# Kernel tuning notes

Hardware: AMD Instinct MI355X
Metric: run time of the kernel (lower is better)

## Reference

```python
import jax, jax.numpy as jnp
import numpy as np

N_NODES = 20000
N_EDGES = 240000
NUM_SPECIES = 4
NUM_BASIS = 16
MAX_RADIUS = 3.15
SQRT_NN = float(np.sqrt(12.0))  # num_neighbors normalization


def _cg121():
    # Clebsch-Gordan for 1e x 2e -> 1e in the real l=2 basis used below:
    # [xy, yz, (3z^2-1), zx, x^2-y^2] (component-normalized). Built from the
    # symmetric traceless matrix pairing M(a) @ v, normalized to unit Frobenius norm.
    s5, s15 = np.sqrt(5.0), np.sqrt(15.0)
    C = np.zeros((3, 5, 3))
    for A in range(5):
        a = np.zeros(5); a[A] = 1.0
        M = np.zeros((3, 3))
        M[0, 1] = M[1, 0] = a[0] * s15 / 2
        M[1, 2] = M[2, 1] = a[1] * s15 / 2
        M[0, 2] = M[2, 0] = a[3] * s15 / 2
        M[0, 0] = -a[2] * s5 / 2 + a[4] * s15 / 2
        M[1, 1] = -a[2] * s5 / 2 - a[4] * s15 / 2
        M[2, 2] = a[2] * s5
        C[:, A, :] = M
    C /= np.linalg.norm(C)
    return jnp.asarray(C, dtype=jnp.float32)

CG121 = _cg121()


def silu(v):
    return v * jax.nn.sigmoid(v)


def lin0(h, W):  # equivariant linear on scalars: [N,u] x [u,v]
    return h @ W / np.sqrt(W.shape[0])


def lin1(h, W):  # equivariant linear on vectors: [N,u,3] x [u,v]
    return jnp.einsum('nuk,uv->nvk', h, W) / np.sqrt(W.shape[0])


def radial_mlp(hb, W1, W2):  # FullyConnectedNet([16,64,nw], silu), normalized weights
    h = silu(hb @ W1 / np.sqrt(W1.shape[0]))
    return h @ W2 / np.sqrt(W2.shape[0])


def radial_basis(r):
    # soft_one_hot_linspace(..., basis='smooth_finite', cutoff=True) * sqrt(NUM_BASIS)
    values = np.linspace(0.0, MAX_RADIUS, NUM_BASIS + 2, dtype=np.float32)[1:-1]
    step = float(values[1] - values[0])
    d = (r[:, None] - values) / step
    def sus(t):
        safe = jnp.where(t > 0, t, 1.0)
        return jnp.where(t > 0, jnp.exp(-1.0 / safe), 0.0)
    y = 1.14136 * float(np.exp(2.0)) * sus(1.0 + d) * sus(1.0 - d)
    return y * np.sqrt(float(NUM_BASIS))


def sph_harm(edge_vec):
    # normalize=True, normalization='component' real spherical harmonics, l=0,1,2
    r = jnp.linalg.norm(edge_vec, axis=1)
    u = edge_vec / r[:, None]
    ux, uy, uz = u[:, 0], u[:, 1], u[:, 2]
    sh1 = np.sqrt(3.0) * u
    sh2 = jnp.stack([np.sqrt(15.0) * ux * uy,
                     np.sqrt(15.0) * uy * uz,
                     np.sqrt(5.0) / 2 * (3 * uz * uz - 1.0),
                     np.sqrt(15.0) * uz * ux,
                     np.sqrt(15.0) / 2 * (ux * ux - uy * uy)], axis=1)
    return r, sh1, sh2


def _forward(x, edge_index, edge_vec, emb,
             L1_lin1_0, L1_W1, L1_W2, L1_lin2_0, L1_lin2_1, L1_sc_0,
             L2_lin1_0, L2_lin1_1, L2_W1, L2_W2, L2_lin2_0, L2_lin2_1, L2_sc_0, L2_sc_1,
             LO_lin1_0, LO_lin1_1, LO_W1, LO_W2, LO_lin2_0, LO_sc_0):
    src, dst = edge_index[0], edge_index[1]
    N = x.shape[0]
    h0 = emb[x]                                   # [N,64] node embedding
    r, sh1, sh2 = sph_harm(edge_vec)
    hb = radial_basis(r)                          # [E,16]

    # ---- interaction 1: 64x0e -> (144x0e + 16x1e) -> gate -> 128x0e + 16x1e
    sc0 = lin0(h0, L1_sc_0)                       # self-connection [N,144]
    x0 = lin0(h0, L1_lin1_0)[src]                 # [E,64]
    w = radial_mlp(hb, L1_W1, L1_W2)              # [E,128] TP weights (uvu)
    m0 = x0 * w[:, :64]                           # 0e x 0e -> 0e
    m1 = (x0 * w[:, 64:128])[:, :, None] * sh1[:, None, :]  # 0e x 1e -> 1e
    a0 = jax.ops.segment_sum(m0, dst, num_segments=N) / SQRT_NN
    a1 = jax.ops.segment_sum(m1, dst, num_segments=N) / SQRT_NN
    g0 = lin0(a0, L1_lin2_0) + sc0                # [N,144]
    g1 = lin1(a1, L1_lin2_1)                      # [N,16,3]
    h0 = silu(g0[:, :128])                        # gated scalars
    h1 = jax.nn.sigmoid(g0[:, 128:])[:, :, None] * g1  # gate 16x1e

    # ---- interaction 2: 128x0e+16x1e -> (144x0e + 176x1e mid) -> gate
    sc0 = lin0(h0, L2_sc_0)                       # [N,144]
    sc1 = lin1(h1, L2_sc_1)                       # [N,16,3]
    x0 = lin0(h0, L2_lin1_0)[src]                 # [E,128]
    x1 = lin1(h1, L2_lin1_1)[src]                 # [E,16,3]
    w = radial_mlp(hb, L2_W1, L2_W2)              # [E,320]
    m0a = x0 * w[:, :128]                                            # 0x0->0
    m0b = jnp.einsum('euk,ek->eu', x1, sh1) / np.sqrt(3.0) * w[:, 272:288]  # 1x1->0
    m1a = (x0 * w[:, 128:256])[:, :, None] * sh1[:, None, :]         # 0x1->1
    m1b = x1 * w[:, 256:272][:, :, None]                             # 1x0->1
    m1c = jnp.cross(x1, sh1[:, None, :]) / np.sqrt(6.0) * w[:, 288:304][:, :, None]  # 1x1->1
    m1d = jnp.einsum('eui,eA,iAk->euk', x1, sh2, CG121) * w[:, 304:320][:, :, None]  # 1x2->1
    mid0 = jnp.concatenate([m0a, m0b], axis=1)    # [E,144]
    mid1 = jnp.concatenate([m1a, m1b, m1c, m1d], axis=1)  # [E,176,3]
    a0 = jax.ops.segment_sum(mid0, dst, num_segments=N) / SQRT_NN
    a1 = jax.ops.segment_sum(mid1, dst, num_segments=N) / SQRT_NN
    g0 = lin0(a0, L2_lin2_0) + sc0
    g1 = lin1(a1, L2_lin2_1) + sc1
    h0 = silu(g0[:, :128])
    h1 = jax.nn.sigmoid(g0[:, 128:])[:, :, None] * g1

    # ---- output interaction: -> 4x0e
    sc0 = lin0(h0, LO_sc_0)                       # [N,4]
    x0 = lin0(h0, LO_lin1_0)[src]
    x1 = lin1(h1, LO_lin1_1)[src]
    w = radial_mlp(hb, LO_W1, LO_W2)              # [E,144]
    m0a = x0 * w[:, :128]
    m0b = jnp.einsum('euk,ek->eu', x1, sh1) / np.sqrt(3.0) * w[:, 128:144]
    a0 = jax.ops.segment_sum(jnp.concatenate([m0a, m0b], axis=1), dst, num_segments=N) / SQRT_NN
    return lin0(a0, LO_lin2_0) + sc0              # [N,4]


def setup_inputs() -> dict:
    key = jax.random.key(0)
    ks = jax.random.split(key, 32)
    f = lambda i, shape: jax.random.normal(ks[i], shape, dtype=jnp.float32)
    return {
        'x': jax.random.randint(ks[0], (N_NODES,), 0, NUM_SPECIES),
        'edge_index': jax.random.randint(ks[1], (2, N_EDGES), 0, N_NODES),
        'edge_vec': jax.random.normal(ks[2], (N_EDGES, 3), dtype=jnp.float32),
        'emb': f(3, (NUM_SPECIES, 64)),
        'L1_lin1_0': f(4, (64, 64)),
        'L1_W1': f(5, (16, 64)), 'L1_W2': f(6, (64, 128)),
        'L1_lin2_0': f(7, (64, 144)), 'L1_lin2_1': f(8, (64, 16)),
        'L1_sc_0': f(9, (64, 144)),
        'L2_lin1_0': f(10, (128, 128)), 'L2_lin1_1': f(11, (16, 16)),
        'L2_W1': f(12, (16, 64)), 'L2_W2': f(13, (64, 320)),
        'L2_lin2_0': f(14, (144, 144)), 'L2_lin2_1': f(15, (176, 16)),
        'L2_sc_0': f(16, (128, 144)), 'L2_sc_1': f(17, (16, 16)),
        'LO_lin1_0': f(18, (128, 128)), 'LO_lin1_1': f(19, (16, 16)),
        'LO_W1': f(20, (16, 64)), 'LO_W2': f(21, (64, 144)),
        'LO_lin2_0': f(22, (144, 4)), 'LO_sc_0': f(23, (128, 4)),
    }


def reference(x, edge_index, edge_vec, emb,
              L1_lin1_0, L1_W1, L1_W2, L1_lin2_0, L1_lin2_1, L1_sc_0,
              L2_lin1_0, L2_lin1_1, L2_W1, L2_W2, L2_lin2_0, L2_lin2_1, L2_sc_0, L2_sc_1,
              LO_lin1_0, LO_lin1_1, LO_W1, LO_W2, LO_lin2_0, LO_sc_0):
    return _forward(x, edge_index, edge_vec, emb,
                    L1_lin1_0, L1_W1, L1_W2, L1_lin2_0, L1_lin2_1, L1_sc_0,
                    L2_lin1_0, L2_lin1_1, L2_W1, L2_W2, L2_lin2_0, L2_lin2_1, L2_sc_0, L2_sc_1,
                    LO_lin1_0, LO_lin1_1, LO_W1, LO_W2, LO_lin2_0, LO_sc_0)
```

## Files before the change

### kernel.cpp

```cpp
#include <hip/hip_runtime.h>
#include <math.h>

#define N_NODES 20000
#define N_EDGES 240000

typedef _Float16 half2_t __attribute__((ext_vector_type(2)));
typedef _Float16 f16x8   __attribute__((ext_vector_type(8)));
typedef float    f32x4v  __attribute__((ext_vector_type(4)));
typedef unsigned uint4v  __attribute__((ext_vector_type(4)));

__device__ __forceinline__ float siluf(float v){ return v * (1.0f/(1.0f+__expf(-v))); }
__device__ __forceinline__ float sigmf(float v){ return 1.0f/(1.0f+__expf(-v)); }

__device__ __forceinline__ unsigned pack_h2(float a, float b){
  half2_t h; h.x = (_Float16)a; h.y = (_Float16)b;
  return __builtin_bit_cast(unsigned, h);
}
__device__ __forceinline__ float dot2f(unsigned w, unsigned h, float acc){
#if __has_builtin(__builtin_amdgcn_fdot2)
  return __builtin_amdgcn_fdot2(__builtin_bit_cast(half2_t,w),
                                __builtin_bit_cast(half2_t,h), acc, false);
#else
  half2_t a = __builtin_bit_cast(half2_t,w), b = __builtin_bit_cast(half2_t,h);
  return acc + (float)a.x*(float)b.x + (float)a.y*(float)b.y;
#endif
}

__global__ void k_count(const int* __restrict__ ei, int* __restrict__ cnt){
  int e = blockIdx.x*blockDim.x + threadIdx.x;
  if (e < N_EDGES) atomicAdd(&cnt[ei[N_EDGES + e]], 1);
}

__global__ void k_scan(const int* __restrict__ cnt, int* __restrict__ off, int* __restrict__ pos){
  __shared__ int part[1024];
  int t = threadIdx.x;
  int c[20]; int s = 0;
  #pragma unroll
  for (int j=0;j<20;j++){
    int idx = t*20 + j;
    int v = (idx < N_NODES) ? cnt[idx] : 0;
    c[j] = s; s += v;
  }
  part[t] = s;
  __syncthreads();
  for (int d=1; d<1024; d<<=1){
    int add = (t>=d) ? part[t-d] : 0;
    __syncthreads();
    part[t] += add;
    __syncthreads();
  }
  int excl = part[t] - s;
  #pragma unroll
  for (int j=0;j<20;j++){
    int idx = t*20 + j;
    if (idx < N_NODES){ off[idx] = excl + c[j]; pos[idx] = excl + c[j]; }
  }
  if (t == 1023) off[N_NODES] = part[1023];
}

__global__ void k_scatter(const int* __restrict__ ei, int* __restrict__ pos,
                          int* __restrict__ perm, int* __restrict__ srcs){
  int e = blockIdx.x*blockDim.x + threadIdx.x;
  if (e >= N_EDGES) return;
  int d = ei[N_EDGES + e];
  int p = atomicAdd(&pos[d], 1);
  perm[e] = p;
  srcs[p] = ei[e];
}

__global__ void k_geom(const float* __restrict__ ev, const int* __restrict__ perm,
                       float* __restrict__ eg){
  int e = blockIdx.x*blockDim.x + threadIdx.x;
  if (e >= N_EDGES) return;
  float x = ev[3*e+0], y = ev[3*e+1], z = ev[3*e+2];
  float r = sqrtf(x*x + y*y + z*z);
  float inv = 1.0f / fmaxf(r, 1e-12f);
  float ux = x*inv, uy = y*inv, uz = z*inv;
  float* o = eg + (size_t)perm[e]*24;
  o[0] = 1.7320508f*ux; o[1] = 1.7320508f*uy; o[2] = 1.7320508f*uz;
  o[3] = 3.8729833f*ux*uy;
  o[4] = 3.8729833f*uy*uz;
  o[5] = 1.1180340f*(3.0f*uz*uz - 1.0f);
  o[6] = 3.8729833f*uz*ux;
  o[7] = 1.9364917f*(ux*ux - uy*uy);
  const float invstep = 17.0f/3.15f;
  float t = r*invstep;
  #pragma unroll
  for (int i=0;i<16;i++){
    float d = t - (float)(i+1);
    float a = 1.0f + d, b = 1.0f - d;
    float v = 0.0f;
    if (a > 0.0f && b > 0.0f) v = 33.734292f*__expf(-1.0f/a - 1.0f/b);
    o[8+i] = v;
  }
}

__global__ void k_packw(const float* __restrict__ W20, const float* __restrict__ Wsc0,
                        const float* __restrict__ Wl0,
                        unsigned* __restrict__ WPu, unsigned* __restrict__ WPs,
                        unsigned* __restrict__ WPl){
  int i = blockIdx.x*blockDim.x + threadIdx.x;
  const float f12 = 1.0f/12.0f;
  const float is128 = 0.08838835f;
  if (i < 144*72){
    int t = i/72, k2 = i%72;
    WPu[i] = pack_h2(W20[(2*k2)*144+t]*f12, W20[(2*k2+1)*144+t]*f12);
  } else if (i < 144*72 + 144*64){
    int ii = i - 144*72; int t = ii/64, k2 = ii%64;
    WPs[ii] = pack_h2(Wsc0[(2*k2)*144+t]*is128, Wsc0[(2*k2+1)*144+t]*is128);
  } else if (i < 144*72 + 144*64 + 128*64){
    int ii = i - 144*72 - 144*64; int t = ii/64, k2 = ii%64;
    WPl[ii] = pack_h2(Wl0[(2*k2)*128+t]*is128, Wl0[(2*k2+1)*128+t]*is128);
  }
}

__global__ void k_node_l1(const int* __restrict__ xs, const float* __restrict__ emb,
                          const float* __restrict__ Wlin, const float* __restrict__ Wsc,
                          float* __restrict__ X0, float* __restrict__ SC0){
  __shared__ float hs[4][64];
  int n0 = blockIdx.x*4;
  int t  = threadIdx.x;
  {
    int j = t>>6, k = t&63;
    hs[j][k] = emb[xs[n0+j]*64 + k];
  }
  __syncthreads();
  if (t < 64){
    float acc[4] = {};
    for (int k=0;k<64;k++){
      float wv = Wlin[k*64 + t];
      #pragma unroll
      for (int j=0;j<4;j++) acc[j] += hs[j][k]*wv;
    }
    #pragma unroll
    for (int j=0;j<4;j++) X0[(size_t)(n0+j)*64 + t] = acc[j]*0.125f;
  } else if (t < 208){
    int o = t - 64;
    float acc[4] = {};
    for (int k=0;k<64;k++){
      float wv = Wsc[k*144 + o];
      #pragma unroll
      for (int j=0;j<4;j++) acc[j] += hs[j][k]*wv;
    }
    #pragma unroll
    for (int j=0;j<4;j++) SC0[(size_t)(n0+j)*144 + o] = acc[j]*0.125f;
  }
}

__global__ __launch_bounds__(256) void k_hidden(
    const float* __restrict__ EG, const float* __restrict__ W1,
    _Float16* __restrict__ H){
  __shared__ float w1s[16*64];
  int tid = threadIdx.x;
  for (int i=tid;i<16*64;i+=256) w1s[i] = W1[i]*0.25f;
  __syncthreads();
  int lane = tid & 63, wib = tid >> 6;
  int gw = blockIdx.x*4 + wib, nw = gridDim.x*4;
  for (int e = gw; e < N_EDGES; e += nw){
    const float* g8 = EG + (size_t)e*24 + 8;
    float a0 = 0.0f, a1 = 0.0f;
    #pragma unroll
    for (int b=0;b<8;b++){
      a0 = fmaf(g8[b],   w1s[b*64 + lane],     a0);
      a1 = fmaf(g8[8+b], w1s[(8+b)*64 + lane], a1);
    }
    H[(size_t)e*64 + lane] = (_Float16)siluf(a0 + a1);
  }
}

template<int MODE>
__device__ __forceinline__ float colscale(int c){
  if constexpr (MODE == 1){
    if (c >= 272 && c < 288) return 0.57735027f;
    if (c >= 288 && c < 304) return 0.40824829f;
    return 1.0f;
  } else if constexpr (MODE == 2){
    return (c >= 128) ? 0.57735027f : 1.0f;
  }
  return 1.0f;
}

template<int NT, int MODE>
__global__ __launch_bounds__(256) void k_ww_mfma(
    int e0c, int e1c, const _Float16* __restrict__ H,
    const float* __restrict__ W2, _Float16* __restrict__ WW){
  constexpr int NCOL = NT*16;
  constexpr int NTW  = (NT + 3) / 4;
  int tid = threadIdx.x;
  int lane = tid & 63, wib = tid >> 6;
  int row = lane & 15, quad = lane >> 4;
  const float fold = 0.125f*0.28867513f;
  f16x8 B0[NTW], B1[NTW];
  #pragma unroll
  for (int t2=0; t2<NTW; t2++){
    int ct = wib*NTW + t2;
    int c  = ct*16 + row;
    bool valid = (ct < NT);
    float fs = valid ? fold*colscale<MODE>(c) : 0.0f;
    int ci = valid ? c : 0;
    #pragma unroll
    for (int j=0;j<8;j++){
      B0[t2][j] = (_Float16)(W2[(quad*8+j)*NCOL + ci]*fs);
      B1[t2][j] = (_Float16)(W2[(32+quad*8+j)*NCOL + ci]*fs);
    }
  }
  int ntiles = (e1c - e0c) >> 4;
  for (int t = blockIdx.x; t < ntiles; t += gridDim.x){
    int eb = e0c + t*16;
    const _Float16* hp = H + (size_t)(eb + row)*64 + quad*8;
    f16x8 A0 = *(const f16x8*)hp;
    f16x8 A1 = *(const f16x8*)(hp + 32);
    #pragma unroll
    for (int t2=0; t2<NTW; t2++){
      int ct = wib*NTW + t2;
      f32x4v d = __builtin_amdgcn_mfma_f32_16x16x32_f16(A0, B0[t2], (f32x4v){0.f,0.f,0.f,0.f}, 0,0,0);
      d = __builtin_amdgcn_mfma_f32_16x16x32_f16(A1, B1[t2], d, 0,0,0);
      if (ct < NT){
        int c0 = ct*16;
        #pragma unroll
        for (int j=0;j<4;j++){
          WW[(size_t)(eb - e0c + quad*4 + j)*NCOL + c0 + row] = (_Float16)d[j];
        }
      }
    }
  }
}

__global__ __launch_bounds__(256) void k_gather_l1(
    const int* __restrict__ off, const int* __restrict__ srcs, const float* __restrict__ eg,
    const _Float16* __restrict__ WW, const float* __restrict__ X0,
    float* __restrict__ A0, float* __restrict__ A1, int e0, int e1, int first){
  int tid = threadIdx.x, lane = tid & 63;
  int gw = (blockIdx.x*256 + tid) >> 6;
  int nw = (gridDim.x*256) >> 6;
  for (int n = gw; n < N_NODES; n += nw){
    int ib = off[n], ie = off[n+1];
    if (ib < e0) ib = e0;
    if (ie > e1) ie = e1;
    if (!first && ib >= ie) continue;
    float a0a = 0.0f, a1a[3] = {0,0,0};
    for (int i = ib; i < ie; i++){
      const float* g = eg + (size_t)i*24;
      const _Float16* w = WW + (size_t)(i - e0)*128;
      float w0  = (float)w[lane];
      float w1v = (float)w[64 + lane];
      float x0 = X0[(size_t)srcs[i]*64 + lane];
      float m0 = x0*w0, m1 = x0*w1v;
      a0a += m0;
      a1a[0] += m1*g[0]; a1a[1] += m1*g[1]; a1a[2] += m1*g[2];
    }
    float* p = A1 + (size_t)n*192 + lane*3;
    if (first){
      A0[(size_t)n*64 + lane] = a0a;
      p[0] = a1a[0]; p[1] = a1a[1]; p[2] = a1a[2];
    } else {
      A0[(size_t)n*64 + lane] += a0a;
      p[0] += a1a[0]; p[1] += a1a[1]; p[2] += a1a[2];
    }
  }
}

__global__ __launch_bounds__(256) void k_gather_l2(
    const int* __restrict__ off, const int* __restrict__ srcs, const float* __restrict__ eg,
    const _Float16* __restrict__ WW, const float* __restrict__ X0, const float* __restrict__ X1,
    float* __restrict__ A0, float* __restrict__ A1, int e0, int e1, int first){
  int tid = threadIdx.x, lane = tid & 63;
  int grp = lane >> 4, v = lane & 15;
  int gw = (blockIdx.x*256 + tid) >> 6;
  int nw = (gridDim.x*256) >> 6;
  for (int n = gw; n < N_NODES; n += nw){
    int ib = off[n], ie = off[n+1];
    if (ib < e0) ib = e0;
    if (ie > e1) ie = e1;
    if (!first && ib >= ie) continue;
    float a0a=0.f, a0b=0.f, a0c=0.f;
    float a1a[3]={0,0,0}, a1b[3]={0,0,0}, a1g[3]={0,0,0};
    for (int i = ib; i < ie; i++){
      const float* g = eg + (size_t)i*24;
      int src = srcs[i];
      const _Float16* w = WW + (size_t)(i - e0)*320;
      float w0  = (float)w[lane];
      float w1v = (float)w[ 64 + lane];
      float w2v = (float)w[128 + lane];
      float w3v = (float)w[192 + lane];
      float w4  = (float)w[256 + lane];
      const float* x0p = X0 + (size_t)src*128;
      float x0a = x0p[lane], x0b = x0p[64 + lane];
      float sx = g[0], sy = g[1], sz = g[2];
      a0a += x0a*w0;
      a0b += x0b*w1v;
      float ma = x0a*w2v, mb = x0b*w3v;
      a1a[0] += ma*sx; a1a[1] += ma*sy; a1a[2] += ma*sz;
      a1b[0] += mb*sx; a1b[1] += mb*sy; a1b[2] += mb*sz;
      const float* x1p = X1 + (size_t)src*48 + v*3;
      float xx = x1p[0], xy = x1p[1], xz = x1p[2];
      if (grp == 0){
        a1g[0] += w4*xx; a1g[1] += w4*xy; a1g[2] += w4*xz;
      } else if (grp == 1){
        a0c += w4*(xx*sx + xy*sy + xz*sz);
      } else if (grp == 2){
        a1g[0] += w4*(xy*sz - xz*sy);
        a1g[1] += w4*(xz*sx - xx*sz);
        a1g[2] += w4*(xx*sy - xy*sx);
      } else {
        float s20=g[3], s21=g[4], s22=g[5], s23=g[6], s24=g[7];
        const float c1c = 0.31622777f, c2c = 0.18257419f;
        a1g[0] += w4*(xx*(c1c*s24 - c2c*s22) + xy*(c1c*s20)            + xz*(c1c*s23));
        a1g[1] += w4*(xx*(c1c*s20)           + xy*(-c2c*s22 - c1c*s24) + xz*(c1c*s21));
        a1g[2] += w4*(xx*(c1c*s23)           + xy*(c1c*s21)            + xz*(2.0f*c2c*s22));
      }
    }
    float* a0 = A0 + (size_t)n*144;
    float* a1 = A1 + (size_t)n*528;
    int gbase = (grp == 0) ? 128 : (grp == 2) ? 144 : (grp == 3) ? 160 : -1;
    if (first){
      a0[lane] = a0a;
      a0[64 + lane] = a0b;
      if (grp == 1) a0[128 + v] = a0c;
      float* p = a1 + lane*3;
      p[0] = a1a[0]; p[1] = a1a[1]; p[2] = a1a[2];
      p = a1 + (64 + lane)*3;
      p[0] = a1b[0]; p[1] = a1b[1]; p[2] = a1b[2];
      if (gbase >= 0){
        p = a1 + (gbase + v)*3;
        p[0] = a1g[0]; p[1] = a1g[1]; p[2] = a1g[2];
      }
    } else {
      a0[lane] += a0a;
      a0[64 + lane] += a0b;
      if (grp == 1) a0[128 + v] += a0c;
      float* p = a1 + lane*3;
      p[0] += a1a[0]; p[1] += a1a[1]; p[2] += a1a[2];
      p = a1 + (64 + lane)*3;
      p[0] += a1b[0]; p[1] += a1b[1]; p[2] += a1b[2];
      if (gbase >= 0){
        p = a1 + (gbase + v)*3;
        p[0] += a1g[0]; p[1] += a1g[1]; p[2] += a1g[2];
      }
    }
  }
}

__global__ __launch_bounds__(256) void k_gather_lo(
    const int* __restrict__ off, const int* __restrict__ srcs, const float* __restrict__ eg,
    const _Float16* __restrict__ WW, const float* __restrict__ X0, const float* __restrict__ X1,
    float* __restrict__ A0, int e0, int e1, int first){
  int tid = threadIdx.x, lane = tid & 63, v = lane & 15;
  int gw = (blockIdx.x*256 + tid) >> 6;
  int nw = (gridDim.x*256) >> 6;
  for (int n = gw; n < N_NODES; n += nw){
    int ib = off[n], ie = off[n+1];
    if (ib < e0) ib = e0;
    if (ie > e1) ie = e1;
    if (!first && ib >= ie) continue;
    float a0a = 0.f, a0b = 0.f, a0c = 0.f;
    for (int i = ib; i < ie; i++){
      const float* g = eg + (size_t)i*24;
      int src = srcs[i];
      const _Float16* w = WW + (size_t)(i - e0)*144;
      float w0  = (float)w[lane];
      float w1v = (float)w[64 + lane];
      float w2v = (float)w[128 + v];
      const float* x0p = X0 + (size_t)src*128;
      a0a += x0p[lane]*w0;
      a0b += x0p[64 + lane]*w1v;
      const float* x1p = X1 + (size_t)src*48 + v*3;
      float dot = x1p[0]*g[0] + x1p[1]*g[1] + x1p[2]*g[2];
      a0c += w2v*dot;
    }
    float* a0 = A0 + (size_t)n*144;
    if (first){
      a0[lane] = a0a;
      a0[64 + lane] = a0b;
      if (lane < 16) a0[128 + lane] = a0c;
    } else {
      a0[lane] += a0a;
      a0[64 + lane] += a0b;
      if (lane < 16) a0[128 + lane] += a0c;
    }
  }
}

__global__ __launch_bounds__(256) void k_upd_l1(
    const float* __restrict__ A0, const float* __restrict__ A1,
    const float* __restrict__ SC0,
    const float* __restrict__ W20, const float* __restrict__ W21,
    float* __restrict__ H0, float* __restrict__ H1){
  __shared__ float a0s[8*64];
  __shared__ float a1s[8*192];
  __shared__ float sig[8][16];
  __shared__ float g1s[8][48];
  int n0 = blockIdx.x*8, t = threadIdx.x;
  {
    const float4* s0 = (const float4*)(A0 + (size_t)n0*64);
    float4* d0 = (float4*)a0s;
    for (int i=t;i<8*64/4;i+=256) d0[i] = s0[i];
    const float4* s1 = (const float4*)(A1 + (size_t)n0*192);
    float4* d1 = (float4*)a1s;
    for (int i=t;i<8*192/4;i+=256) d1[i] = s1[i];
  }
  __syncthreads();
  if (t < 144){
    float acc[8] = {};
    for (int k=0;k<64;k++){
      float wv = W20[k*144 + t];
      #pragma unroll
      for (int j=0;j<8;j++) acc[j] += a0s[j*64 + k]*wv;
    }
    #pragma unroll
    for (int j=0;j<8;j++){
      float gg = acc[j]*0.125f + SC0[(size_t)(n0+j)*144 + t];
      if (t < 128) H0[(size_t)(n0+j)*128 + t] = siluf(gg);
      else         sig[j][t-128] = sigmf(gg);
    }
  } else if (t < 192){
    int idx = t-144, v = idx/3, k = idx%3;
    float acc[8] = {};
    for (int u=0;u<64;u++){
      float wv = W21[u*16 + v];
      #pragma unroll
      for (int j=0;j<8;j++) acc[j] += a1s[j*192 + u*3 + k]*wv;
    }
    #pragma unroll
    for (int j=0;j<8;j++) g1s[j][idx] = acc[j]*0.125f;
  }
  __syncthreads();
  if (t >= 144 && t < 192){
    int idx = t-144, v = idx/3;
    #pragma unroll
    for (int j=0;j<8;j++) H1[(size_t)(n0+j)*48 + idx] = sig[j][v]*g1s[j][idx];
  }
}

__global__ __launch_bounds__(384) void k_lin_l2(
    const float* __restrict__ H0, const float* __restrict__ H1,
    const unsigned* __restrict__ WPs, const float* __restrict__ Wsc1,
    const unsigned* __restrict__ WPl, const float* __restrict__ Wl1,
    float* __restrict__ SC0, float* __restrict__ SC1,
    float* __restrict__ X0,  float* __restrict__ X1){
  __shared__ uint4v h0h8[128];
  __shared__ float h1s[8*48];
  int n0 = blockIdx.x*8, t = threadIdx.x;
  if (t < 128){
    const float4* s0 = (const float4*)(H0 + (size_t)n0*128);
    float4 f0 = s0[t*2], f1 = s0[t*2+1];
    uint4v u;
    u.x = pack_h2(f0.x, f0.y); u.y = pack_h2(f0.z, f0.w);
    u.z = pack_h2(f1.x, f1.y); u.w = pack_h2(f1.z, f1.w);
    h0h8[t] = u;
  } else if (t < 224){
    int i = t - 128;
    const float4* s1 = (const float4*)(H1 + (size_t)n0*48);
    if (i < 96) ((float4*)h1s)[i] = s1[i];
  }
  __syncthreads();
  const uint4v* wps4 = (const uint4v*)WPs;
  const uint4v* wpl4 = (const uint4v*)WPl;
  if (t < 144){
    float acc[8] = {};
    for (int kq=0;kq<16;kq++){
      uint4v wq = wps4[t*16 + kq];
      #pragma unroll
      for (int j=0;j<8;j++){
        uint4v av = h0h8[j*16 + kq];
        acc[j] = dot2f(wq.x, av.x, acc[j]);
        acc[j] = dot2f(wq.y, av.y, acc[j]);
        acc[j] = dot2f(wq.z, av.z, acc[j]);
        acc[j] = dot2f(wq.w, av.w, acc[j]);
      }
    }
    #pragma unroll
    for (int j=0;j<8;j++) SC0[(size_t)(n0+j)*144 + t] = acc[j];
  } else if (t < 192){
    int idx = t-144, v = idx/3, k = idx%3;
    float acc[8] = {};
    for (int u=0;u<16;u++){
      float wv = Wsc1[u*16 + v];
      #pragma unroll
      for (int j=0;j<8;j++) acc[j] += h1s[j*48 + u*3 + k]*wv;
    }
    #pragma unroll
    for (int j=0;j<8;j++) SC1[(size_t)(n0+j)*48 + idx] = acc[j]*0.25f;
  } else if (t < 320){
    int o = t-192;
    float acc[8] = {};
    for (int kq=0;kq<16;kq++){
      uint4v wq = wpl4[o*16 + kq];
      #pragma unroll
      for (int j=0;j<8;j++){
        uint4v av = h0h8[j*16 + kq];
        acc[j] = dot2f(wq.x, av.x, acc[j]);
        acc[j] = dot2f(wq.y, av.y, acc[j]);
        acc[j] = dot2f(wq.z, av.z, acc[j]);
        acc[j] = dot2f(wq.w, av.w, acc[j]);
      }
    }
    #pragma unroll
    for (int j=0;j<8;j++) X0[(size_t)(n0+j)*128 + o] = acc[j];
  } else if (t < 368){
    int idx = t-320, v = idx/3, k = idx%3;
    float acc[8] = {};
    for (int u=0;u<16;u++){
      float wv = Wl1[u*16 + v];
      #pragma unroll
      for (int j=0;j<8;j++) acc[j] += h1s[j*48 + u*3 + k]*wv;
    }
    #pragma unroll
    for (int j=0;j<8;j++) X1[(size_t)(n0+j)*48 + idx] = acc[j]*0.25f;
  }
}

__global__ __launch_bounds__(256) void k_upd_l2(
    const float* __restrict__ A0, const float* __restrict__ A1,
    const float* __restrict__ SC0, const float* __restrict__ SC1,
    const unsigned* __restrict__ WPu, const float* __restrict__ W21,
    float* __restrict__ H0, float* __restrict__ H1){
  __shared__ uint4v a0h8[144];
  __shared__ float a1s[8*528];
  __shared__ float sig[8][16];
  __shared__ float g1s[8][48];
  int n0 = blockIdx.x*8, t = threadIdx.x;
  if (t < 144){
    const float4* s0 = (const float4*)(A0 + (size_t)n0*144);
    float4 f0 = s0[t*2], f1 = s0[t*2+1];
    uint4v u;
    u.x = pack_h2(f0.x, f0.y); u.y = pack_h2(f0.z, f0.w);
    u.z = pack_h2(f1.x, f1.y); u.w = pack_h2(f1.z, f1.w);
    a0h8[t] = u;
  }
  {
    const float4* s1 = (const float4*)(A1 + (size_t)n0*528);
    float4* d1 = (float4*)a1s;
    for (int i=t;i<8*528/4;i+=256) d1[i] = s1[i];
  }
  __syncthreads();
  const uint4v* wpu4 = (const uint4v*)WPu;
  if (t < 144){
    float acc[8] = {};
    for (int kq=0;kq<18;kq++){
      uint4v wq = wpu4[t*18 + kq];
      #pragma unroll
      for (int j=0;j<8;j++){
        uint4v av = a0h8[j*18 + kq];
        acc[j] = dot2f(wq.x, av.x, acc[j]);
        acc[j] = dot2f(wq.y, av.y, acc[j]);
        acc[j] = dot2f(wq.z, av.z, acc[j]);
        acc[j] = dot2f(wq.w, av.w, acc[j]);
      }
    }
    #pragma unroll
    for (int j=0;j<8;j++){
      float gg = acc[j] + SC0[(size_t)(n0+j)*144 + t];
      if (t < 128) H0[(size_t)(n0+j)*128 + t] = siluf(gg);
      else         sig[j][t-128] = sigmf(gg);
    }
  } else if (t < 192){
    int idx = t-144, v = idx/3, k = idx%3;
    float acc[8] = {};
    for (int u=0;u<176;u++){
      float wv = W21[u*16 + v];
      #pragma unroll
      for (int j=0;j<8;j++) acc[j] += a1s[j*528 + u*3 + k]*wv;
    }
    #pragma unroll
    for (int j=0;j<8;j++) g1s[j][idx] = acc[j]*0.075377836f + SC1[(size_t)(n0+j)*48 + idx];
  }
  __syncthreads();
  if (t >= 144 && t < 192){
    int idx = t-144, v = idx/3;
    #pragma unroll
    for (int j=0;j<8;j++) H1[(size_t)(n0+j)*48 + idx] = sig[j][v]*g1s[j][idx];
  }
}

__global__ __launch_bounds__(256) void k_lin_lo(
    const float* __restrict__ H0, const float* __restrict__ H1,
    const float* __restrict__ Wsc0,
    const float* __restrict__ Wl0, const float* __restrict__ Wl1,
    float* __restrict__ SCO, float* __restrict__ X0, float* __restrict__ X1){
  __shared__ float h0s[8*128];
  __shared__ float h1s[8*48];
  int n0 = blockIdx.x*8, t = threadIdx.x;
  {
    const float4* s0 = (const float4*)(H0 + (size_t)n0*128);
    float4* d0 = (float4*)h0s;
    for (int i=t;i<8*128/4;i+=256) d0[i] = s0[i];
    const float4* s1 = (const float4*)(H1 + (size_t)n0*48);
    float4* d1 = (float4*)h1s;
    for (int i=t;i<8*48/4;i+=256) d1[i] = s1[i];
  }
  __syncthreads();
  const float is128 = 0.08838835f;
  if (t < 4){
    float acc[8] = {};
    for (int k=0;k<128;k++){
      float wv = Wsc0[k*4 + t];
      #pragma unroll
      for (int j=0;j<8;j++) acc[j] += h0s[j*128 + k]*wv;
    }
    #pragma unroll
    for (int j=0;j<8;j++) SCO[(size_t)(n0+j)*4 + t] = acc[j]*is128;
  } else if (t < 132){
    int o = t-4;
    float acc[8] = {};
    for (int k=0;k<128;k++){
      float wv = Wl0[k*128 + o];
      #pragma unroll
      for (int j=0;j<8;j++) acc[j] += h0s[j*128 + k]*wv;
    }
    #pragma unroll
    for (int j=0;j<8;j++) X0[(size_t)(n0+j)*128 + o] = acc[j]*is128;
  } else if (t < 180){
    int idx = t-132, v = idx/3, k = idx%3;
    float acc[8] = {};
    for (int u=0;u<16;u++){
      float wv = Wl1[u*16 + v];
      #pragma unroll
      for (int j=0;j<8;j++) acc[j] += h1s[j*48 + u*3 + k]*wv;
    }
    #pragma unroll
    for (int j=0;j<8;j++) X1[(size_t)(n0+j)*48 + idx] = acc[j]*0.25f;
  }
}

__global__ __launch_bounds__(256) void k_final(
    const float* __restrict__ A0, const float* __restrict__ SCO,
    const float* __restrict__ W, float* __restrict__ out){
  __shared__ float a0s[8*144];
  int n0 = blockIdx.x*8, t = threadIdx.x;
  {
    const float4* s0 = (const float4*)(A0 + (size_t)n0*144);
    float4* d0 = (float4*)a0s;
    for (int i=t;i<8*144/4;i+=256) d0[i] = s0[i];
  }
  __syncthreads();
  if (t < 32){
    int j = t >> 2, c = t & 3;
    float acc = 0.0f;
    for (int k=0;k<144;k++) acc += a0s[j*144 + k]*W[k*4 + c];
    int i = (n0 + j)*4 + c;
    out[i] = acc*(1.0f/12.0f) + SCO[i];
  }
}

extern "C" void kernel_launch(void* const* d_in, const int* in_sizes, int n_in,
                              void* d_out, int out_size, void* d_ws, size_t ws_size,
                              hipStream_t stream) {
  const int*   x   = (const int*)  d_in[0];
  const int*   ei  = (const int*)  d_in[1];
  const float* ev  = (const float*)d_in[2];
  const float* emb = (const float*)d_in[3];
  const float* L1_lin1_0 = (const float*)d_in[4];
  const float* L1_W1     = (const float*)d_in[5];
  const float* L1_W2     = (const float*)d_in[6];
  const float* L1_lin2_0 = (const float*)d_in[7];
  const float* L1_lin2_1 = (const float*)d_in[8];
  const float* L1_sc_0   = (const float*)d_in[9];
  const float* L2_lin1_0 = (const float*)d_in[10];
  const float* L2_lin1_1 = (const float*)d_in[11];
  const float* L2_W1     = (const float*)d_in[12];
  const float* L2_W2     = (const float*)d_in[13];
  const float* L2_lin2_0 = (const float*)d_in[14];
  const float* L2_lin2_1 = (const float*)d_in[15];
  const float* L2_sc_0   = (const float*)d_in[16];
  const float* L2_sc_1   = (const float*)d_in[17];
  const float* LO_lin1_0 = (const float*)d_in[18];
  const float* LO_lin1_1 = (const float*)d_in[19];
  const float* LO_W1     = (const float*)d_in[20];
  const float* LO_W2     = (const float*)d_in[21];
  const float* LO_lin2_0 = (const float*)d_in[22];
  const float* LO_sc_0   = (const float*)d_in[23];
  float* out = (float*)d_out;

  int* cnt  = (int*)d_ws;
  int* off  = cnt  + N_NODES;
  int* pos  = off  + N_NODES + 1;
  int* perm = pos  + N_NODES;
  int* srcs = perm + N_EDGES;
  float* EG  = (float*)(((char*)d_ws) + ((size_t)540004 * 4));
  float* X0  = EG  + (size_t)N_EDGES*24;
  float* X1  = X0  + (size_t)N_NODES*128;
  float* SC0 = X1  + (size_t)N_NODES*48;
  float* SC1 = SC0 + (size_t)N_NODES*144;
  float* A0  = SC1 + (size_t)N_NODES*48;
  float* A1  = A0  + (size_t)N_NODES*144;
  float* H0  = A1  + (size_t)N_NODES*528;
  float* H1  = H0  + (size_t)N_NODES*128;
  _Float16* HH = (_Float16*)(H1 + (size_t)N_NODES*48);
  unsigned* WPu = (unsigned*)(HH + (size_t)N_EDGES*64);
  unsigned* WPs = WPu + 144*72;
  unsigned* WPl = WPs + 144*64;
  _Float16* WW = (_Float16*)(WPl + 128*64);

  size_t used = (size_t)((char*)WW - (char*)d_ws);
  size_t avail = (ws_size > used) ? (ws_size - used) : 0;
  auto chunk_for = [&](int ncol)->int{
    size_t ce = avail / ((size_t)ncol * sizeof(_Float16));
    if (ce >= (size_t)N_EDGES) return N_EDGES;
    int c = (int)ce & ~15;
    return c < 4096 ? 4096 : c;
  };

  hipMemsetAsync(cnt, 0, N_NODES*sizeof(int), stream);
  k_count  <<<(N_EDGES+255)/256, 256, 0, stream>>>(ei, cnt);
  k_scan   <<<1, 1024, 0, stream>>>(cnt, off, pos);
  k_scatter<<<(N_EDGES+255)/256, 256, 0, stream>>>(ei, pos, perm, srcs);
  k_geom   <<<(N_EDGES+255)/256, 256, 0, stream>>>(ev, perm, EG);
  k_packw  <<<109, 256, 0, stream>>>(L2_lin2_0, L2_sc_0, L2_lin1_0, WPu, WPs, WPl);

  k_node_l1<<<N_NODES/4, 256, 0, stream>>>(x, emb, L1_lin1_0, L1_sc_0, X0, SC0);
  k_hidden<<<2048, 256, 0, stream>>>(EG, L1_W1, HH);
  {
    int chunk = chunk_for(128);
    for (int e0 = 0; e0 < N_EDGES; e0 += chunk){
      int e1 = (e0 + chunk < N_EDGES) ? e0 + chunk : N_EDGES;
      k_ww_mfma<8,0><<<2048, 256, 0, stream>>>(e0, e1, HH, L1_W2, WW);
      k_gather_l1<<<2500, 256, 0, stream>>>(off, srcs, EG, WW, X0, A0, A1, e0, e1, e0==0);
    }
  }
  k_upd_l1<<<N_NODES/8, 256, 0, stream>>>(A0, A1, SC0, L1_lin2_0, L1_lin2_1, H0, H1);

  k_lin_l2<<<N_NODES/8, 384, 0, stream>>>(H0, H1, WPs, L2_sc_1, WPl, L2_lin1_1,
                                          SC0, SC1, X0, X1);
  k_hidden<<<2048, 256, 0, stream>>>(EG, L2_W1, HH);
  {
    int chunk = chunk_for(320);
    for (int e0 = 0; e0 < N_EDGES; e0 += chunk){
      int e1 = (e0 + chunk < N_EDGES) ? e0 + chunk : N_EDGES;
      k_ww_mfma<20,1><<<2048, 256, 0, stream>>>(e0, e1, HH, L2_W2, WW);
      k_gather_l2<<<2500, 256, 0, stream>>>(off, srcs, EG, WW, X0, X1, A0, A1, e0, e1, e0==0);
    }
  }
  k_upd_l2<<<N_NODES/8, 256, 0, stream>>>(A0, A1, SC0, SC1, WPu, L2_lin2_1, H0, H1);

  k_lin_lo<<<N_NODES/8, 256, 0, stream>>>(H0, H1, LO_sc_0, LO_lin1_0, LO_lin1_1, SC1, X0, X1);
  k_hidden<<<2048, 256, 0, stream>>>(EG, LO_W1, HH);
  {
    int chunk = chunk_for(144);
    for (int e0 = 0; e0 < N_EDGES; e0 += chunk){
      int e1 = (e0 + chunk < N_EDGES) ? e0 + chunk : N_EDGES;
      k_ww_mfma<9,2><<<2048, 256, 0, stream>>>(e0, e1, HH, LO_W2, WW);
      k_gather_lo<<<2500, 256, 0, stream>>>(off, srcs, EG, WW, X0, X1, A0, e0, e1, e0==0);
    }
  }
  k_final<<<N_NODES/8, 256, 0, stream>>>(A0, SC1, LO_lin2_0, out);
}
```

Baseline: 677.5 us.

## Fuse layer-2 radial weight MFMA into the gather kernel via shared memory

Replaces the chunked pair of kernels for layer 2 (an MFMA kernel writing per-edge weights to global memory, then a gather kernel reading them) with one kernel. Each block handles four destination nodes, computes the per-edge 320-wide weights for 16-edge tiles with MFMA into LDS, and gathers from LDS. This removes the global round-trip of the large per-edge weight buffer and the extra launches from chunking. In exchange, each block reloads and converts W2 into registers, adds block-level syncs per tile, and degree imbalance across the four nodes in a block can leave waves idle.

New measurement: 733.5 us. +8.3%, slower.

```diff
diff --git a/kernel.cpp b/kernel.cpp
--- a/kernel.cpp
+++ b/kernel.cpp
@@ -226,64 +226,60 @@
   }
 }
 
-__global__ __launch_bounds__(256) void k_gather_l1(
-    const int* __restrict__ off, const int* __restrict__ srcs, const float* __restrict__ eg,
-    const _Float16* __restrict__ WW, const float* __restrict__ X0,
-    float* __restrict__ A0, float* __restrict__ A1, int e0, int e1, int first){
-  int tid = threadIdx.x, lane = tid & 63;
-  int gw = (blockIdx.x*256 + tid) >> 6;
-  int nw = (gridDim.x*256) >> 6;
-  for (int n = gw; n < N_NODES; n += nw){
-    int ib = off[n], ie = off[n+1];
-    if (ib < e0) ib = e0;
-    if (ie > e1) ie = e1;
-    if (!first && ib >= ie) continue;
-    float a0a = 0.0f, a1a[3] = {0,0,0};
-    for (int i = ib; i < ie; i++){
-      const float* g = eg + (size_t)i*24;
-      const _Float16* w = WW + (size_t)(i - e0)*128;
-      float w0  = (float)w[lane];
-      float w1v = (float)w[64 + lane];
-      float x0 = X0[(size_t)srcs[i]*64 + lane];
-      float m0 = x0*w0, m1 = x0*w1v;
-      a0a += m0;
-      a1a[0] += m1*g[0]; a1a[1] += m1*g[1]; a1a[2] += m1*g[2];
-    }
-    float* p = A1 + (size_t)n*192 + lane*3;
-    if (first){
-      A0[(size_t)n*64 + lane] = a0a;
-      p[0] = a1a[0]; p[1] = a1a[1]; p[2] = a1a[2];
-    } else {
-      A0[(size_t)n*64 + lane] += a0a;
-      p[0] += a1a[0]; p[1] += a1a[1]; p[2] += a1a[2];
-    }
-  }
-}
-
-__global__ __launch_bounds__(256) void k_gather_l2(
-    const int* __restrict__ off, const int* __restrict__ srcs, const float* __restrict__ eg,
-    const _Float16* __restrict__ WW, const float* __restrict__ X0, const float* __restrict__ X1,
-    float* __restrict__ A0, float* __restrict__ A1, int e0, int e1, int first){
-  int tid = threadIdx.x, lane = tid & 63;
+__global__ __launch_bounds__(256) void k_fused_l2(
+    const int* __restrict__ off, const int* __restrict__ srcs,
+    const float* __restrict__ eg, const _Float16* __restrict__ H,
+    const float* __restrict__ W2,
+    const float* __restrict__ X0, const float* __restrict__ X1,
+    float* __restrict__ A0, float* __restrict__ A1){
+  __shared__ _Float16 wws[16][322];
+  int tid = threadIdx.x;
+  int lane = tid & 63, wib = tid >> 6;
+  int row = lane & 15, quad = lane >> 4;
   int grp = lane >> 4, v = lane & 15;
-  int gw = (blockIdx.x*256 + tid) >> 6;
-  int nw = (gridDim.x*256) >> 6;
-  for (int n = gw; n < N_NODES; n += nw){
-    int ib = off[n], ie = off[n+1];
-    if (ib < e0) ib = e0;
-    if (ie > e1) ie = e1;
-    if (!first && ib >= ie) continue;
-    float a0a=0.f, a0b=0.f, a0c=0.f;
-    float a1a[3]={0,0,0}, a1b[3]={0,0,0}, a1g[3]={0,0,0};
-    for (int i = ib; i < ie; i++){
+  const float fold = 0.125f*0.28867513f;
+  f16x8 B0[5], B1[5];
+  #pragma unroll
+  for (int t2=0; t2<5; t2++){
+    int c = (wib*5 + t2)*16 + row;
+    float fs = fold*colscale<1>(c);
+    #pragma unroll
+    for (int j=0;j<8;j++){
+      B0[t2][j] = (_Float16)(W2[(quad*8+j)*320 + c]*fs);
+      B1[t2][j] = (_Float16)(W2[(32+quad*8+j)*320 + c]*fs);
+    }
+  }
+  int n0 = blockIdx.x*4;
+  int gb0 = off[n0], gb1 = off[n0+4];
+  int ib = off[n0+wib], ie = off[n0+wib+1];
+  float a0a=0.f, a0b=0.f, a0c=0.f;
+  float a1a[3]={0,0,0}, a1b[3]={0,0,0}, a1g[3]={0,0,0};
+  for (int tb = gb0; tb < gb1; tb += 16){
+    const _Float16* hp = H + (size_t)(tb + row)*64 + quad*8;
+    f16x8 Af0 = *(const f16x8*)hp;
+    f16x8 Af1 = *(const f16x8*)(hp + 32);
+    #pragma unroll
+    for (int t2=0; t2<5; t2++){
+      f32x4v d = __builtin_amdgcn_mfma_f32_16x16x32_f16(Af0, B0[t2], (f32x4v){0.f,0.f,0.f,0.f}, 0,0,0);
+      d = __builtin_amdgcn_mfma_f32_16x16x32_f16(Af1, B1[t2], d, 0,0,0);
+      int c0 = (wib*5 + t2)*16;
+      #pragma unroll
+      for (int j=0;j<4;j++){
+        wws[quad*4 + j][c0 + row] = (_Float16)d[j];
+      }
+    }
+    __syncthreads();
+    int lo = (ib > tb) ? ib : tb;
+    int hi = (ie < tb+16) ? ie : tb+16;
+    for (int i = lo; i < hi; i++){
+      int r = i - tb;
       const float* g = eg + (size_t)i*24;
       int src = srcs[i];
-      const _Float16* w = WW + (size_t)(i - e0)*320;
-      float w0  = (float)w[lane];
-      float w1v = (float)w[ 64 + lane];
-      float w2v = (float)w[128 + lane];
-      float w3v = (float)w[192 + lane];
-      float w4  = (float)w[256 + lane];
+      float w0  = (float)wws[r][lane];
+      float w1v = (float)wws[r][ 64 + lane];
+      float w2v = (float)wws[r][128 + lane];
+      float w3v = (float)wws[r][192 + lane];
+      float w4  = (float)wws[r][256 + lane];
       const float* x0p = X0 + (size_t)src*128;
       float x0a = x0p[lane], x0b = x0p[64 + lane];
       float sx = g[0], sy = g[1], sz = g[2];
@@ -310,33 +306,55 @@
         a1g[2] += w4*(xx*(c1c*s23)           + xy*(c1c*s21)            + xz*(2.0f*c2c*s22));
       }
     }
-    float* a0 = A0 + (size_t)n*144;
-    float* a1 = A1 + (size_t)n*528;
-    int gbase = (grp == 0) ? 128 : (grp == 2) ? 144 : (grp == 3) ? 160 : -1;
+    __syncthreads();
+  }
+  int n = n0 + wib;
+  float* a0 = A0 + (size_t)n*144;
+  float* a1 = A1 + (size_t)n*528;
+  a0[lane] = a0a;
+  a0[64 + lane] = a0b;
+  if (grp == 1) a0[128 + v] = a0c;
+  float* p = a1 + lane*3;
+  p[0] = a1a[0]; p[1] = a1a[1]; p[2] = a1a[2];
+  p = a1 + (64 + lane)*3;
+  p[0] = a1b[0]; p[1] = a1b[1]; p[2] = a1b[2];
+  int gbase = (grp == 0) ? 128 : (grp == 2) ? 144 : (grp == 3) ? 160 : -1;
+  if (gbase >= 0){
+    p = a1 + (gbase + v)*3;
+    p[0] = a1g[0]; p[1] = a1g[1]; p[2] = a1g[2];
+  }
+}
+
+__global__ __launch_bounds__(256) void k_gather_l1(
+    const int* __restrict__ off, const int* __restrict__ srcs, const float* __restrict__ eg,
+    const _Float16* __restrict__ WW, const float* __restrict__ X0,
+    float* __restrict__ A0, float* __restrict__ A1, int e0, int e1, int first){
+  int tid = threadIdx.x, lane = tid & 63;
+  int gw = (blockIdx.x*256 + tid) >> 6;
+  int nw = (gridDim.x*256) >> 6;
+  for (int n = gw; n < N_NODES; n += nw){
+    int ib = off[n], ie = off[n+1];
+    if (ib < e0) ib = e0;
+    if (ie > e1) ie = e1;
+    if (!first && ib >= ie) continue;
+    float a0a = 0.0f, a1a[3] = {0,0,0};
+    for (int i = ib; i < ie; i++){
+      const float* g = eg + (size_t)i*24;
+      const _Float16* w = WW + (size_t)(i - e0)*128;
+      float w0  = (float)w[lane];
+      float w1v = (float)w[64 + lane];
+      float x0 = X0[(size_t)srcs[i]*64 + lane];
+      float m0 = x0*w0, m1 = x0*w1v;
+      a0a += m0;
+      a1a[0] += m1*g[0]; a1a[1] += m1*g[1]; a1a[2] += m1*g[2];
+    }
+    float* p = A1 + (size_t)n*192 + lane*3;
     if (first){
-      a0[lane] = a0a;
-      a0[64 + lane] = a0b;
-      if (grp == 1) a0[128 + v] = a0c;
-      float* p = a1 + lane*3;
+      A0[(size_t)n*64 + lane] = a0a;
       p[0] = a1a[0]; p[1] = a1a[1]; p[2] = a1a[2];
-      p = a1 + (64 + lane)*3;
-      p[0] = a1b[0]; p[1] = a1b[1]; p[2] = a1b[2];
-      if (gbase >= 0){
-        p = a1 + (gbase + v)*3;
-        p[0] = a1g[0]; p[1] = a1g[1]; p[2] = a1g[2];
-      }
     } else {
-      a0[lane] += a0a;
-      a0[64 + lane] += a0b;
-      if (grp == 1) a0[128 + v] += a0c;
-      float* p = a1 + lane*3;
+      A0[(size_t)n*64 + lane] += a0a;
       p[0] += a1a[0]; p[1] += a1a[1]; p[2] += a1a[2];
-      p = a1 + (64 + lane)*3;
-      p[0] += a1b[0]; p[1] += a1b[1]; p[2] += a1b[2];
-      if (gbase >= 0){
-        p = a1 + (gbase + v)*3;
-        p[0] += a1g[0]; p[1] += a1g[1]; p[2] += a1g[2];
-      }
     }
   }
 }
@@ -723,14 +741,7 @@
   k_lin_l2<<<N_NODES/8, 384, 0, stream>>>(H0, H1, WPs, L2_sc_1, WPl, L2_lin1_1,
                                           SC0, SC1, X0, X1);
   k_hidden<<<2048, 256, 0, stream>>>(EG, L2_W1, HH);
-  {
-    int chunk = chunk_for(320);
-    for (int e0 = 0; e0 < N_EDGES; e0 += chunk){
-      int e1 = (e0 + chunk < N_EDGES) ? e0 + chunk : N_EDGES;
-      k_ww_mfma<20,1><<<2048, 256, 0, stream>>>(e0, e1, HH, L2_W2, WW);
-      k_gather_l2<<<2500, 256, 0, stream>>>(off, srcs, EG, WW, X0, X1, A0, A1, e0, e1, e0==0);
-    }
-  }
+  k_fused_l2<<<N_NODES/4, 256, 0, stream>>>(off, srcs, EG, HH, L2_W2, X0, X1, A0, A1);
   k_upd_l2<<<N_NODES/8, 256, 0, stream>>>(A0, A1, SC0, SC1, WPu, L2_lin2_1, H0, H1);
 
   k_lin_lo<<<N_NODES/8, 256, 0, stream>>>(H0, H1, LO_sc_0, LO_lin1_0, LO_lin1_1, SC1, X0, X1);
```
